# Kernel optimization log

Measured on AMD Instinct MI355X. Metric: run time of the kernel, lower is better.

The kernel has to match this reference:

```python
import jax, jax.numpy as jnp
import numpy as np
import math

NUM_HEADS = 16
HEAVY_RATIO = 0.1
RECENT_RATIO = 0.1
ROPE_THETA = 10000.0


def setup_inputs() -> dict:
    key = jax.random.key(0)
    ks = jax.random.split(key, 5)
    b, s, h = 1, 2048, 2048
    return {
        "hidden_states": jax.random.normal(ks[0], (b, s, h), dtype=jnp.float32),
        "Wq": jax.random.normal(ks[1], (h, h), dtype=jnp.float32) * 0.02,
        "Wk": jax.random.normal(ks[2], (h, h), dtype=jnp.float32) * 0.02,
        "Wv": jax.random.normal(ks[3], (h, h), dtype=jnp.float32) * 0.02,
        "Wo": jax.random.normal(ks[4], (h, h), dtype=jnp.float32) * 0.02,
    }


def _rotate_half(x):
    d = x.shape[-1]
    return jnp.concatenate([-x[..., d // 2:], x[..., : d // 2]], axis=-1)


def _rope(q, k, seq_len, head_dim, dtype):
    # LLaMA rotary embedding: inv_freq over even dims, emb = [freqs, freqs]
    inv_freq = 1.0 / (ROPE_THETA ** (jnp.arange(0, head_dim, 2, dtype=jnp.float32) / head_dim))
    pos = jnp.arange(seq_len, dtype=jnp.float32)
    freqs = pos[:, None] * inv_freq[None, :]            # [s, d/2]
    emb = jnp.concatenate([freqs, freqs], axis=-1)       # [s, d]
    cos = jnp.cos(emb).astype(dtype)[None, None]         # [1,1,s,d]
    sin = jnp.sin(emb).astype(dtype)[None, None]
    q = q * cos + _rotate_half(q) * sin
    k = k * cos + _rotate_half(k) * sin
    return q, k


def reference(hidden_states, Wq, Wk, Wv, Wo):
    b, s, hidden = hidden_states.shape
    H = NUM_HEADS
    d = hidden // H

    def proj(W):  # nn.Linear(x) = x @ W.T, then split heads -> [b,H,s,d]
        return (hidden_states @ W.T).reshape(b, s, H, d).transpose(0, 2, 1, 3)

    q, k, v = proj(Wq), proj(Wk), proj(Wv)
    q, k = _rope(q, k, s, d, hidden_states.dtype)

    scores = jnp.einsum("bhqd,bhkd->bhqk", q, k) / math.sqrt(d)  # [b,H,s,s]
    neg = jnp.finfo(scores.dtype).min
    i = jnp.arange(s)[:, None]
    j = jnp.arange(s)[None, :]
    causal = jnp.where(j <= i, jnp.array(0.0, scores.dtype), neg)
    scores = jnp.maximum(scores + causal, neg)

    heavy_budget = int(HEAVY_RATIO * s)
    recent_budget = int(RECENT_RATIO * s)

    # first softmax (fp32), accumulate column importances
    tmp_attn = jax.nn.softmax(scores.astype(jnp.float32), axis=-1).astype(scores.dtype)
    tmp_sum = jnp.sum(tmp_attn, axis=-2)                 # [b,H,s]
    _, topk_idx = jax.lax.top_k(tmp_sum, heavy_budget)   # [b,H,heavy]
    heavy_mask = jnp.any(topk_idx[..., :, None] == jnp.arange(s)[None, None, None, :], axis=-2)  # [b,H,s]

    # recent band: tril(diag=recent) & triu(diag=-recent)  <=>  |i-j| <= recent
    band = jnp.abs(i - j) <= recent_budget               # [s,s]
    mask = heavy_mask[:, :, None, :] | band[None, None]

    scores = jnp.where(mask, scores, neg)
    probs = jax.nn.softmax(scores.astype(jnp.float32), axis=-1).astype(q.dtype)
    attn = jnp.einsum("bhqk,bhkd->bhqd", probs, v)
    attn = attn.transpose(0, 2, 1, 3).reshape(b, s, hidden)
    return attn @ Wo.T
```

## Files before the change

kernel.cpp:

```cpp
#include <hip/hip_runtime.h>
#include <hip/hip_bf16.h>
#include <stdint.h>

#define SEQ   2048
#define HIDN  2048
#define NHEAD 16
#define HDIM  128
#define HEAVY 204
#define RECENT 204

typedef __attribute__((ext_vector_type(4))) float f32x4;
typedef __attribute__((ext_vector_type(8))) short bf16x8;
typedef unsigned short u16;
typedef unsigned int   u32;

static __device__ __forceinline__ u16 f2bf(float f){
  union { float f; u32 u; } v; v.f = f;
  u32 r = (v.u + 0x7FFFu + ((v.u >> 16) & 1u)) >> 16;
  return (u16)r;
}
static __device__ __forceinline__ float bf2f(u16 u){
  union { u32 u; float f; } v; v.u = ((u32)u) << 16;
  return v.f;
}

static __device__ __forceinline__ void gload16(const void* g, void* l){
  __builtin_amdgcn_global_load_lds((const __attribute__((address_space(1))) u32*)g,
                                   (__attribute__((address_space(3))) u32*)l, 16, 0, 0);
}

#define WAITVM(N) asm volatile("s_waitcnt vmcnt(" #N ")" ::: "memory")
#define BARRAW    __builtin_amdgcn_s_barrier()
#define PRIO1     __builtin_amdgcn_s_setprio(1)
#define PRIO0     __builtin_amdgcn_s_setprio(0)

static __device__ __forceinline__ void stage_tile(const u16* __restrict__ base, size_t stride,
                                                  int row0, u16* __restrict__ lds, int tid){
  const int wbase = tid & ~63;
#pragma unroll
  for (int it = 0; it < 4; ++it){
    int m = it * 256 + tid;
    int row = m >> 4, cp = m & 15;
    gload16(base + (size_t)(row0 + row) * stride + ((cp ^ (row & 7)) * 8),
            lds + (it * 256 + wbase) * 8);
  }
}

__global__ void k_prep(const float* __restrict__ A0, const float* __restrict__ A1,
                       const float* __restrict__ A2, const float* __restrict__ A3,
                       const float* __restrict__ A4, u16* __restrict__ out,
                       float* __restrict__ cosT, float* __restrict__ sinT,
                       float* __restrict__ colsum){
  int b = blockIdx.x, tid = threadIdx.x;
  if (b < 20480){
    int id = b * 256 + tid;
    int sel = id >> 20, off = (id & 1048575) * 4;
    const float* src = sel == 0 ? A0 : sel == 1 ? A1 : sel == 2 ? A2 : sel == 3 ? A3 : A4;
    float4 v = *(const float4*)(src + off);
    ushort4 o;
    o.x = f2bf(v.x); o.y = f2bf(v.y); o.z = f2bf(v.z); o.w = f2bf(v.w);
    *(ushort4*)(out + (size_t)sel * 4194304 + off) = o;
  } else if (b < 20992){
    int i = (b - 20480) * 256 + tid;
    int pos = i >> 6, j = i & 63;
    float invf = powf(10000.0f, -(float)j * (1.0f / 64.0f));
    float a = (float)pos * invf;
    cosT[i] = cosf(a);
    sinT[i] = sinf(a);
  } else {
    int i = (b - 20992) * 256 + tid;
    if (i < 16384) ((float4*)colsum)[i] = (float4){0.f, 0.f, 0.f, 0.f};
  }
}

__global__ void k_post(u16* __restrict__ Qm, u16* __restrict__ Km,
                       const float* __restrict__ cosT, const float* __restrict__ sinT,
                       const u16* __restrict__ V, u16* __restrict__ Vt){
  __shared__ u16 t[32][33];
  int b = blockIdx.x, tid = threadIdx.x;
  if (b < 4096){
    int gid = b * 256 + tid;
    u16* M = (gid < 524288) ? Qm : Km;
    int id = gid & 524287;
    int pos = id >> 8, rem = id & 255;
    int h = rem >> 4, j4 = (rem & 15) * 4;
    u16* p = M + (size_t)pos * HIDN + h * HDIM + j4;
    ushort4 lo = *(ushort4*)p;
    ushort4 hi = *(ushort4*)(p + 64);
    float4 c = *(const float4*)(cosT + pos * 64 + j4);
    float4 s = *(const float4*)(sinT + pos * 64 + j4);
    float l0 = bf2f(lo.x), l1 = bf2f(lo.y), l2 = bf2f(lo.z), l3 = bf2f(lo.w);
    float h0 = bf2f(hi.x), h1 = bf2f(hi.y), h2 = bf2f(hi.z), h3 = bf2f(hi.w);
    ushort4 nlo, nhi;
    nlo.x = f2bf(l0 * c.x - h0 * s.x);  nhi.x = f2bf(h0 * c.x + l0 * s.x);
    nlo.y = f2bf(l1 * c.y - h1 * s.y);  nhi.y = f2bf(h1 * c.y + l1 * s.y);
    nlo.z = f2bf(l2 * c.z - h2 * s.z);  nhi.z = f2bf(h2 * c.z + l2 * s.z);
    nlo.w = f2bf(l3 * c.w - h3 * s.w);  nhi.w = f2bf(h3 * c.w + l3 * s.w);
    *(ushort4*)p = nlo;
    *(ushort4*)(p + 64) = nhi;
  } else {
    int b2 = b - 4096;
    int s0 = (b2 & 63) * 32, c0 = (b2 >> 6) * 32;
    int r = tid >> 3, cc = (tid & 7) * 4;
    ushort4 v = *(const ushort4*)(V + (size_t)(s0 + r) * 2048 + c0 + cc);
    t[r][cc] = v.x; t[r][cc + 1] = v.y; t[r][cc + 2] = v.z; t[r][cc + 3] = v.w;
    __syncthreads();
    int co = tid >> 3, ro = (tid & 7) * 4;
    ushort4 o;
    o.x = t[ro][co]; o.y = t[ro + 1][co]; o.z = t[ro + 2][co]; o.w = t[ro + 3][co];
    *(ushort4*)(Vt + (size_t)(c0 + co) * 2048 + s0 + ro) = o;
  }
}

__global__ __launch_bounds__(512, 1)
void k_g256(const u16* __restrict__ X, const u16* __restrict__ Wq, const u16* __restrict__ Wk,
            const u16* __restrict__ Wv, u16* __restrict__ C0, u16* __restrict__ C1,
            u16* __restrict__ C2){
  __shared__ __align__(16) u16 LA[2][256 * 64];
  __shared__ __align__(16) u16 LB[2][192 * 64];
  const int tid = threadIdx.x;
  const int lane = tid & 63, wvi = tid >> 6;
  const int wm = wvi >> 2, wn = wvi & 3;
  const int g = lane >> 4, c15 = lane & 15;
  const int brow = blockIdx.y * 256;
  const int bcol = blockIdx.x * 192;
  const int NT = 32;

  f32x4 acc[8][3];
#pragma unroll
  for (int m = 0; m < 8; m++)
#pragma unroll
    for (int n = 0; n < 3; n++) acc[m][n] = (f32x4){0.f, 0.f, 0.f, 0.f};

  const int cc0 = ((g ^ (c15 & 7)) * 8);
  bf16x8 af[4][2], bf[3][2];

#define BPTR(rB_) (rB_ < 2048 ? Wq + (size_t)(rB_) * 2048 \
                 : rB_ < 4096 ? Wk + (size_t)((rB_) - 2048) * 2048 \
                              : Wv + (size_t)((rB_) - 4096) * 2048)
#define STGA(grow0, gcol0, ldsb) do { \
  _Pragma("unroll") for (int it = 0; it < 2; ++it){ \
    int m_ = it * 512 + tid; \
    int row_ = m_ >> 3, cp_ = m_ & 7; \
    gload16(X + (size_t)((grow0) + row_) * 2048 + (gcol0) + ((cp_ ^ (row_ & 7)) * 8), \
            (ldsb) + (it * 512 + (tid & ~63)) * 8); \
  } } while(0)
#define STGB128(gcol0, ldsb) do { \
  _Pragma("unroll") for (int it = 0; it < 2; ++it){ \
    int m_ = it * 512 + tid; \
    int row_ = m_ >> 3, cp_ = m_ & 7; \
    int rB_ = bcol + row_; \
    const u16* bp_ = BPTR(rB_); \
    gload16(bp_ + (gcol0) + ((cp_ ^ (row_ & 7)) * 8), \
            (ldsb) + (it * 512 + (tid & ~63)) * 8); \
  } } while(0)
#define STGB64(gcol0, ldsb) do { \
    int row_ = 128 + (tid >> 3), cp_ = tid & 7; \
    int rB_ = bcol + row_; \
    const u16* bp_ = BPTR(rB_); \
    gload16(bp_ + (gcol0) + ((cp_ ^ (row_ & 7)) * 8), \
            (ldsb) + (tid & ~63) * 8); \
  } while(0)
#define RDA(buf, mibase) \
  _Pragma("unroll") for (int mi2 = 0; mi2 < 4; ++mi2){ \
    const u16* pr = &LA[buf][0] + (size_t)(wm * 128 + ((mibase) + mi2) * 16 + c15) * 64; \
    af[mi2][0] = *(const bf16x8*)(pr + cc0); \
    af[mi2][1] = *(const bf16x8*)(pr + (cc0 ^ 32)); \
  }
#define RDB2(buf) \
  _Pragma("unroll") for (int ni2 = 0; ni2 < 2; ++ni2){ \
    const u16* pr = &LB[buf][0] + (size_t)(wn * 48 + ni2 * 16 + c15) * 64; \
    bf[ni2][0] = *(const bf16x8*)(pr + cc0); \
    bf[ni2][1] = *(const bf16x8*)(pr + (cc0 ^ 32)); \
  }
#define RDB1(buf) do { \
    const u16* pr = &LB[buf][0] + (size_t)(wn * 48 + 32 + c15) * 64; \
    bf[2][0] = *(const bf16x8*)(pr + cc0); \
    bf[2][1] = *(const bf16x8*)(pr + (cc0 ^ 32)); \
  } while(0)
#define MM2(mibase) \
  _Pragma("unroll") for (int mi2 = 0; mi2 < 4; ++mi2) \
  _Pragma("unroll") for (int ni2 = 0; ni2 < 2; ++ni2) \
  _Pragma("unroll") for (int kk = 0; kk < 2; ++kk) \
    acc[(mibase) + mi2][ni2] = __builtin_amdgcn_mfma_f32_16x16x32_bf16( \
        af[mi2][kk], bf[ni2][kk], acc[(mibase) + mi2][ni2], 0, 0, 0);
#define MM1(mibase) \
  _Pragma("unroll") for (int mi2 = 0; mi2 < 4; ++mi2) \
  _Pragma("unroll") for (int kk = 0; kk < 2; ++kk) \
    acc[(mibase) + mi2][2] = __builtin_amdgcn_mfma_f32_16x16x32_bf16( \
        af[mi2][kk], bf[2][kk], acc[(mibase) + mi2][2], 0, 0, 0);

  STGA(brow,       0, &LA[0][0]);
  STGA(brow + 128, 0, &LA[0][0] + 128 * 64);
  STGB128(0,  &LB[0][0]);
  STGB64(0,   &LB[0][0] + 128 * 64);
  STGB128(64, &LB[1][0]);
  STGB64(64,  &LB[1][0] + 128 * 64);
  WAITVM(3);
  BARRAW;

  for (int t = 0; t < NT; t += 2){
    const int kn1 = (t + 1) * 64;
    const int kn2 = (t + 2) * 64;
    const int kn3 = (t + 3) * 64;
    RDA(0, 0); RDB2(0);
    STGA(brow, kn1, &LA[1][0]);
    BARRAW; PRIO1; MM2(0); PRIO0; BARRAW;
    RDB1(0);
    STGA(brow + 128, kn1, &LA[1][0] + 128 * 64);
    BARRAW; PRIO1; MM1(0); PRIO0; BARRAW;
    RDA(0, 4);
    if (t + 2 < NT) STGB128(kn2, &LB[0][0]);
    BARRAW; PRIO1; MM1(4); PRIO0; BARRAW;
    if (t + 2 < NT){ STGB64(kn2, &LB[0][0] + 128 * 64); WAITVM(3); }
    else            { WAITVM(0); }
    BARRAW; PRIO1; MM2(4); PRIO0; BARRAW;
    RDA(1, 0); RDB2(1);
    if (t + 2 < NT) STGA(brow, kn2, &LA[0][0]);
    BARRAW; PRIO1; MM2(0); PRIO0; BARRAW;
    RDB1(1);
    if (t + 2 < NT) STGA(brow + 128, kn2, &LA[0][0] + 128 * 64);
    BARRAW; PRIO1; MM1(0); PRIO0; BARRAW;
    RDA(1, 4);
    if (t + 3 < NT) STGB128(kn3, &LB[1][0]);
    BARRAW; PRIO1; MM1(4); PRIO0; BARRAW;
    if (t + 3 < NT){ STGB64(kn3, &LB[1][0] + 128 * 64); WAITVM(3); }
    else if (t + 2 < NT){ WAITVM(0); }
    BARRAW; PRIO1; MM2(4); PRIO0; BARRAW;
  }
#undef BPTR
#undef STGA
#undef STGB128
#undef STGB64
#undef RDA
#undef RDB2
#undef RDB1
#undef MM2
#undef MM1

#pragma unroll
  for (int mi = 0; mi < 8; ++mi)
#pragma unroll
    for (int ni = 0; ni < 3; ++ni){
      int colbase = bcol + wn * 48 + ni * 16;
      int proj = colbase >> 11;
      u16* Cb = proj == 0 ? C0 : proj == 1 ? C1 : C2;
      int lc = (colbase & 2047) + c15;
#pragma unroll
      for (int r = 0; r < 4; ++r){
        int row = brow + wm * 128 + mi * 16 + g * 4 + r;
        Cb[(size_t)row * 2048 + lc] = f2bf(acc[mi][ni][r]);
      }
    }
}

static __device__ __forceinline__ void stage_g(const u16* __restrict__ A, const u16* __restrict__ B,
                                               int brow, int bcol, int k0,
                                               u16* __restrict__ as, u16* __restrict__ bs, int tid){
  const int wbase = tid & ~63;
#pragma unroll
  for (int it = 0; it < 2; ++it){
    int m = it * 256 + tid;
    int row = m >> 2, q = m & 3;
    gload16(A + (size_t)(brow + row) * 2048 + k0 + q * 8, as + (it * 256 + wbase) * 8);
    gload16(B + (size_t)(bcol + row) * 2048 + k0 + q * 8, bs + (it * 256 + wbase) * 8);
  }
}

__global__ __launch_bounds__(256)
void k_gemm_out(const u16* __restrict__ A, const u16* __restrict__ B, float* __restrict__ C){
  __shared__ __align__(16) u16 As[2][128 * 32];
  __shared__ __align__(16) u16 Bs[2][128 * 32];
  const int tid = threadIdx.x;
  const int w = tid >> 6, lane = tid & 63;
  const int wr = w >> 1, wc = w & 1;
  const int g = lane >> 4, c15 = lane & 15;
  const int brow = blockIdx.y * 128, bcol = blockIdx.x * 128;

  f32x4 acc[4][4];
#pragma unroll
  for (int m = 0; m < 4; m++)
#pragma unroll
    for (int n = 0; n < 4; n++) acc[m][n] = (f32x4){0.f, 0.f, 0.f, 0.f};

  stage_g(A, B, brow, bcol, 0, As[0], Bs[0], tid);
  int cur = 0;
  for (int kt = 0; kt < 64; ++kt){
    if (kt + 1 < 64){ stage_g(A, B, brow, bcol, (kt + 1) * 32, As[cur ^ 1], Bs[cur ^ 1], tid);
                      WAITVM(4); }
    else            { WAITVM(0); }
    BARRAW;
    bf16x8 af[4], bfr[4];
#pragma unroll
    for (int m = 0; m < 4; m++) af[m] = *(const bf16x8*)(As[cur] + (wr * 64 + m * 16 + c15) * 32 + g * 8);
#pragma unroll
    for (int n = 0; n < 4; n++) bfr[n] = *(const bf16x8*)(Bs[cur] + (wc * 64 + n * 16 + c15) * 32 + g * 8);
    PRIO1;
#pragma unroll
    for (int m = 0; m < 4; m++)
#pragma unroll
      for (int n = 0; n < 4; n++)
        acc[m][n] = __builtin_amdgcn_mfma_f32_16x16x32_bf16(af[m], bfr[n], acc[m][n], 0, 0, 0);
    PRIO0;
    BARRAW;
    cur ^= 1;
  }
#pragma unroll
  for (int m = 0; m < 4; m++)
#pragma unroll
    for (int n = 0; n < 4; n++)
#pragma unroll
      for (int r = 0; r < 4; r++){
        int row = brow + wr * 64 + m * 16 + g * 4 + r;
        int col = bcol + wc * 64 + n * 16 + c15;
        C[(size_t)row * 2048 + col] = acc[m][n][r];
      }
}

__global__ __launch_bounds__(256)
void k_pass1a(const u16* __restrict__ Q, const u16* __restrict__ K, float* __restrict__ rowsum){
  __shared__ __align__(16) u16 Ks[2][64 * 128];
  const int tid = threadIdx.x;
  const int wv = tid >> 6, lane = tid & 63;
  const int g = lane >> 4, c15 = lane & 15;
  const int h = blockIdx.y;
  int qb = 0, c = 0;
  { int rem = blockIdx.x; int q = 0;
    while (rem >= ((2 * q + 9) >> 3)){ rem -= (2 * q + 9) >> 3; q++; }
    qb = q; c = rem; }
  const int i0 = qb * 128;
  const int ktend = 2 * qb + 2;
  const int kt0 = c * 8;
  const int kt1 = (ktend < kt0 + 8) ? ktend : (kt0 + 8);
  const u16* Qh = Q + h * HDIM;
  const u16* Kh = K + h * HDIM;
  const float scale = 0.08838834764831845f;
  const int wb = wv * 32;

  bf16x8 qfr[2][4];
#pragma unroll
  for (int m = 0; m < 2; m++)
#pragma unroll
    for (int ks = 0; ks < 4; ks++)
      qfr[m][ks] = *(const bf16x8*)(Qh + (size_t)(i0 + wb + m * 16 + c15) * 2048 + ks * 32 + g * 8);

  stage_tile(Kh, 2048, kt0 * 64, Ks[0], tid);

  float rs[2][4] = {{0.f,0.f,0.f,0.f},{0.f,0.f,0.f,0.f}};
  int cur = 0;
  for (int kt = kt0; kt < kt1; ++kt){
    if (kt + 1 < kt1){ stage_tile(Kh, 2048, (kt + 1) * 64, Ks[cur ^ 1], tid); WAITVM(4); }
    else             { WAITVM(0); }
    BARRAW;
    const int k0 = kt * 64;
    f32x4 sacc[2][4];
#pragma unroll
    for (int m = 0; m < 2; m++)
#pragma unroll
      for (int n = 0; n < 4; n++) sacc[m][n] = (f32x4){0.f, 0.f, 0.f, 0.f};
#pragma unroll
    for (int ks = 0; ks < 4; ++ks){
#pragma unroll
      for (int n = 0; n < 4; n++){
        int brw = n * 16 + c15;
        bf16x8 b = *(const bf16x8*)(Ks[cur] + brw * 128 + ((ks * 32 + g * 8) ^ ((brw & 7) << 3)));
#pragma unroll
        for (int m = 0; m < 2; m++)
          sacc[m][n] = __builtin_amdgcn_mfma_f32_16x16x32_bf16(qfr[m][ks], b, sacc[m][n], 0, 0, 0);
      }
    }
    if (kt < 2 * qb){
#pragma unroll
      for (int m = 0; m < 2; m++)
#pragma unroll
        for (int n = 0; n < 4; n++)
#pragma unroll
          for (int r = 0; r < 4; r++)
            rs[m][r] += __expf(sacc[m][n][r] * scale);
    } else {
#pragma unroll
      for (int n = 0; n < 4; n++){
        int col = k0 + n * 16 + c15;
#pragma unroll
        for (int m = 0; m < 2; m++)
#pragma unroll
          for (int r = 0; r < 4; r++){
            int rowg = i0 + wb + m * 16 + g * 4 + r;
            rs[m][r] += (col <= rowg) ? __expf(sacc[m][n][r] * scale) : 0.f;
          }
      }
    }
    BARRAW;
    cur ^= 1;
  }
#pragma unroll
  for (int m = 0; m < 2; m++)
#pragma unroll
    for (int r = 0; r < 4; r++){
      float v = rs[m][r];
      v += __shfl_xor(v, 1); v += __shfl_xor(v, 2);
      v += __shfl_xor(v, 4); v += __shfl_xor(v, 8);
      if (c15 == 0)
        atomicAdd(&rowsum[h * 2048 + i0 + wb + m * 16 + g * 4 + r], v);
    }
}

__global__ __launch_bounds__(256)
void k_pass1b(const u16* __restrict__ Q, const u16* __restrict__ K,
              const float* __restrict__ rowsum, float* __restrict__ colsum){
  __shared__ __align__(16) u16 Qs[2][64 * 128];
  const int tid = threadIdx.x;
  const int wv = tid >> 6, lane = tid & 63;
  const int g = lane >> 4, c15 = lane & 15;
  const int h = blockIdx.y;
  int kb = 0, c = 0;
  { int rem = blockIdx.x; int q = 0;
    while (rem >= ((39 - 2 * q) >> 3)){ rem -= (39 - 2 * q) >> 3; q++; }
    kb = q; c = rem; }
  const int k0 = kb * 128;
  const int qt0 = 2 * kb + c * 8;
  const int qt1 = (2 * kb + c * 8 + 8 < 32) ? (2 * kb + c * 8 + 8) : 32;
  const u16* Qh = Q + h * HDIM;
  const u16* Kh = K + h * HDIM;
  const float scale = 0.08838834764831845f;
  const int wb = wv * 32;
  const float* rsrow = rowsum + h * 2048;

  bf16x8 kfr[2][4];
#pragma unroll
  for (int m = 0; m < 2; m++)
#pragma unroll
    for (int ks = 0; ks < 4; ks++)
      kfr[m][ks] = *(const bf16x8*)(Kh + (size_t)(k0 + wb + m * 16 + c15) * 2048 + ks * 32 + g * 8);

  stage_tile(Qh, 2048, qt0 * 64, Qs[0], tid);

  float racc[2][4] = {{0.f,0.f,0.f,0.f},{0.f,0.f,0.f,0.f}};
  int cur = 0;
  for (int qt = qt0; qt < qt1; ++qt){
    if (qt + 1 < qt1){ stage_tile(Qh, 2048, (qt + 1) * 64, Qs[cur ^ 1], tid); WAITVM(4); }
    else             { WAITVM(0); }
    BARRAW;
    const int i0q = qt * 64;
    float rw[4];
#pragma unroll
    for (int n = 0; n < 4; n++)
      rw[n] = 1.0f / rsrow[i0q + n * 16 + c15];
    f32x4 sacc[2][4];
#pragma unroll
    for (int m = 0; m < 2; m++)
#pragma unroll
      for (int n = 0; n < 4; n++) sacc[m][n] = (f32x4){0.f, 0.f, 0.f, 0.f};
#pragma unroll
    for (int ks = 0; ks < 4; ++ks){
#pragma unroll
      for (int n = 0; n < 4; n++){
        int brw = n * 16 + c15;
        bf16x8 b = *(const bf16x8*)(Qs[cur] + brw * 128 + ((ks * 32 + g * 8) ^ ((brw & 7) << 3)));
#pragma unroll
        for (int m = 0; m < 2; m++)
          sacc[m][n] = __builtin_amdgcn_mfma_f32_16x16x32_bf16(kfr[m][ks], b, sacc[m][n], 0, 0, 0);
      }
    }
    if (qt >= 2 * kb + 2){
#pragma unroll
      for (int m = 0; m < 2; m++)
#pragma unroll
        for (int n = 0; n < 4; n++)
#pragma unroll
          for (int r = 0; r < 4; r++)
            racc[m][r] += __expf(sacc[m][n][r] * scale) * rw[n];
    } else {
#pragma unroll
      for (int n = 0; n < 4; n++){
        int colq = i0q + n * 16 + c15;
#pragma unroll
        for (int m = 0; m < 2; m++)
#pragma unroll
          for (int r = 0; r < 4; r++){
            int rowk = k0 + wb + m * 16 + g * 4 + r;
            racc[m][r] += (rowk <= colq) ? __expf(sacc[m][n][r] * scale) * rw[n] : 0.f;
          }
      }
    }
    BARRAW;
    cur ^= 1;
  }
#pragma unroll
  for (int m = 0; m < 2; m++)
#pragma unroll
    for (int r = 0; r < 4; r++){
      float v = racc[m][r];
      v += __shfl_xor(v, 1); v += __shfl_xor(v, 2);
      v += __shfl_xor(v, 4); v += __shfl_xor(v, 8);
      if (c15 == 0)
        atomicAdd(&colsum[h * 2048 + k0 + wb + m * 16 + g * 4 + r], v);
    }
}

__global__ __launch_bounds__(1024)
void k_topk(const float* __restrict__ colsum, short* __restrict__ cidx){
  __shared__ float v[2048];
  __shared__ short ix[2048];
  __shared__ short sx[256];
  const int tid = threadIdx.x;
  const int h = blockIdx.x;
  for (int i = tid; i < 2048; i += 1024){ v[i] = colsum[h * 2048 + i]; ix[i] = (short)i; }
  __syncthreads();
  for (int k = 2; k <= 2048; k <<= 1){
    for (int j = k >> 1; j > 0; j >>= 1){
      int i = ((tid / j) * (j << 1)) + (tid % j);
      int l = i + j;
      float vi = v[i], vl = v[l];
      short ii = ix[i], il = ix[l];
      bool before_i = (vi > vl) || (vi == vl && ii < il);
      bool dir = (i & k) == 0;
      if (dir ? !before_i : before_i){ v[i] = vl; v[l] = vi; ix[i] = il; ix[l] = ii; }
      __syncthreads();
    }
  }
  if (tid < 256) sx[tid] = (tid < HEAVY) ? ix[tid] : (short)32767;
  __syncthreads();
  for (int k = 2; k <= 256; k <<= 1){
    for (int j = k >> 1; j > 0; j >>= 1){
      if (tid < 128){
        int i = ((tid / j) * (j << 1)) + (tid % j);
        int l = i + j;
        short a = sx[i], b = sx[l];
        bool asc = (i & k) == 0;
        if (asc ? (a > b) : (a < b)){ sx[i] = b; sx[l] = a; }
      }
      __syncthreads();
    }
  }
  if (tid < 256) cidx[h * 256 + tid] = sx[tid];
}

__global__ void k_gatherKV(const u16* __restrict__ Kb, const u16* __restrict__ Vb,
                           const short* __restrict__ cidx,
                           u16* __restrict__ Kg, u16* __restrict__ Vg){
  __shared__ __align__(16) u16 t[32][136];
  int b = blockIdx.x, tid = threadIdx.x;
  if (b < 256){
    int gid = b * 256 + tid;
    int h = gid >> 12, rem = gid & 4095;
    int slot = rem >> 4, cp = rem & 15;
    int cid = cidx[h * 256 + slot];
    bf16x8 z = (bf16x8){0,0,0,0,0,0,0,0};
    bf16x8 val = (cid < 2048) ? *(const bf16x8*)(Kb + (size_t)cid * 2048 + h * 128 + cp * 8) : z;
    *(bf16x8*)(Kg + ((size_t)h * 256 + slot) * 128 + cp * 8) = val;
  } else {
    int b2 = b - 256;
    int h = b2 >> 3, s0 = (b2 & 7) * 32;
#pragma unroll
    for (int it = 0; it < 2; ++it){
      int m = it * 256 + tid;
      int s = m >> 4, cp = m & 15;
      int cid = cidx[h * 256 + s0 + s];
      bf16x8 z = (bf16x8){0,0,0,0,0,0,0,0};
      bf16x8 val = (cid < 2048) ? *(const bf16x8*)(Vb + (size_t)cid * 2048 + h * 128 + cp * 8) : z;
      *(bf16x8*)(&t[s][cp * 8]) = val;
    }
    __syncthreads();
#pragma unroll
    for (int i = 0; i < 16; ++i){
      int idx = i * 256 + tid;
      int d = idx >> 5, s = idx & 31;
      Vg[((size_t)h * 128 + d) * 256 + s0 + s] = t[s][d];
    }
  }
}

static __device__ __forceinline__ void load_vf(const u16* __restrict__ Vt,
                                               const u16* __restrict__ Vg,
                                               int h, int e, int g, int c15,
                                               bf16x8 vf[2][8]){
  const bool isg = (e >= 100);
#pragma unroll
  for (int ks2 = 0; ks2 < 2; ++ks2)
#pragma unroll
    for (int f = 0; f < 8; ++f){
      int vrow = f * 16 + c15;
      vf[ks2][f] = isg
        ? *(const bf16x8*)(Vg + ((size_t)h * 128 + vrow) * 256 + (e - 100) * 64 + ks2 * 32 + g * 8)
        : *(const bf16x8*)(Vt + ((size_t)h * 128 + vrow) * 2048 + e * 64 + ks2 * 32 + g * 8);
    }
}

__global__ __launch_bounds__(256)
void k_pass2(const u16* __restrict__ Q, const u16* __restrict__ K, const u16* __restrict__ Vt,
             const u16* __restrict__ Kg, const u16* __restrict__ Vg,
             const short* __restrict__ cidx, u16* __restrict__ attn){
  __shared__ __align__(16) u16 Qs[64 * 128];
  __shared__ __align__(16) u16 Ks[2][64 * 128];
  __shared__ __align__(16) u16 Ps[4][16 * 64];
  __shared__ short cids[256];
  __shared__ int lists[12];
  __shared__ int nact_s;
  const int tid = threadIdx.x;
  const int w = tid >> 6, lane = tid & 63;
  const int g = lane >> 4, c15 = lane & 15;
  const int qb = blockIdx.x, h = blockIdx.y;
  const int i0 = qb * 64;
  const u16* Qh = Q + h * HDIM;
  const u16* Kh = K + h * HDIM;
  const u16* Kgh = Kg + (size_t)h * 256 * 128;
  const float scale = 0.08838834764831845f;
  const int arow = w * 16 + c15;

  if (tid < 256) cids[tid] = cidx[h * 256 + tid];
  __syncthreads();
  if (tid == 0){
    int n = 0;
    int ktb0 = (i0 > RECENT) ? ((i0 - RECENT) >> 6) : 0;
    for (int kt = ktb0; kt <= qb; ++kt) lists[n++] = kt;
    for (int gt = 0; gt < 4; ++gt)
      if ((int)cids[gt * 64] <= i0 - RECENT + 62) lists[n++] = 100 + gt;
    nact_s = n;
  }
  __syncthreads();
  const int nact = nact_s;

  stage_tile(Qh, 2048, i0, Qs, tid);
  { int e = lists[0];
    if (e < 100) stage_tile(Kh, 2048, e * 64, Ks[0], tid);
    else         stage_tile(Kgh, 128, (e - 100) * 64, Ks[0], tid); }
  bf16x8 vf[2][8];
  load_vf(Vt, Vg, h, lists[0], g, c15, vf);
  WAITVM(16);
  BARRAW;

  f32x4 oacc[8];
#pragma unroll
  for (int f = 0; f < 8; f++) oacc[f] = (f32x4){0.f, 0.f, 0.f, 0.f};
  float lsum[4] = {0.f, 0.f, 0.f, 0.f};

  int cur = 0;
  for (int i = 0; i < nact; ++i){
    const int e = lists[i];
    const bool isg = (e >= 100);
    const bool nxt = (i + 1 < nact);
    if (nxt){
      int e2 = lists[i + 1];
      if (e2 < 100) stage_tile(Kh, 2048, e2 * 64, Ks[cur ^ 1], tid);
      else          stage_tile(Kgh, 128, (e2 - 100) * 64, Ks[cur ^ 1], tid);
      WAITVM(20);
    } else {
      WAITVM(16);
    }
    BARRAW;
    f32x4 sacc[4];
#pragma unroll
    for (int n = 0; n < 4; n++) sacc[n] = (f32x4){0.f, 0.f, 0.f, 0.f};
#pragma unroll
    for (int ks = 0; ks < 4; ++ks){
      bf16x8 a = *(const bf16x8*)(Qs + arow * 128 + ((ks * 32 + g * 8) ^ ((arow & 7) << 3)));
#pragma unroll
      for (int n = 0; n < 4; n++){
        int brw = n * 16 + c15;
        bf16x8 b = *(const bf16x8*)(Ks[cur] + brw * 128 + ((ks * 32 + g * 8) ^ ((brw & 7) << 3)));
        sacc[n] = __builtin_amdgcn_mfma_f32_16x16x32_bf16(a, b, sacc[n], 0, 0, 0);
      }
    }
#pragma unroll
    for (int n = 0; n < 4; n++){
      int cid = isg ? (int)cids[(e - 100) * 64 + n * 16 + c15] : (e * 64 + n * 16 + c15);
#pragma unroll
      for (int r = 0; r < 4; r++){
        int rowg = i0 + w * 16 + g * 4 + r;
        int dist = rowg - cid;
        bool valid = (cid <= rowg) && (isg ? (dist > RECENT) : (dist <= RECENT));
        float ev = valid ? __expf(sacc[n][r] * scale) : 0.f;
        lsum[r] += ev;
        int prow = g * 4 + r;
        Ps[w][prow * 64 + ((n * 16 + c15) ^ ((prow & 7) << 3))] = f2bf(ev);
      }
    }
    if (nxt) WAITVM(4); else WAITVM(0);
    PRIO1;
#pragma unroll
    for (int ks2 = 0; ks2 < 2; ++ks2){
      bf16x8 pa = *(const bf16x8*)(&Ps[w][c15 * 64 + ((ks2 * 32 + g * 8) ^ ((c15 & 7) << 3))]);
#pragma unroll
      for (int f = 0; f < 8; ++f)
        oacc[f] = __builtin_amdgcn_mfma_f32_16x16x32_bf16(pa, vf[ks2][f], oacc[f], 0, 0, 0);
    }
    PRIO0;
    if (nxt) load_vf(Vt, Vg, h, lists[i + 1], g, c15, vf);
    BARRAW;
    cur ^= 1;
  }
  float rinv[4];
#pragma unroll
  for (int r = 0; r < 4; r++){
    float v = lsum[r];
    v += __shfl_xor(v, 1); v += __shfl_xor(v, 2);
    v += __shfl_xor(v, 4); v += __shfl_xor(v, 8);
    rinv[r] = 1.0f / v;
  }
#pragma unroll
  for (int f = 0; f < 8; f++)
#pragma unroll
    for (int r = 0; r < 4; r++){
      int rowg = i0 + w * 16 + g * 4 + r;
      attn[(size_t)rowg * 2048 + h * HDIM + f * 16 + c15] = f2bf(oacc[f][r] * rinv[r]);
    }
}

extern "C" void kernel_launch(void* const* d_in, const int* in_sizes, int n_in,
                              void* d_out, int out_size, void* d_ws, size_t ws_size,
                              hipStream_t stream){
  const float* X  = (const float*)d_in[0];
  const float* Wq = (const float*)d_in[1];
  const float* Wk = (const float*)d_in[2];
  const float* Wv = (const float*)d_in[3];
  const float* Wo = (const float*)d_in[4];

  char* w = (char*)d_ws;
  const size_t MB8 = (size_t)2048 * 2048 * 2;
  u16* Xb  = (u16*)(w);
  u16* Wqb = (u16*)(w + 1 * MB8);
  u16* Wkb = (u16*)(w + 2 * MB8);
  u16* Wvb = (u16*)(w + 3 * MB8);
  u16* Wob = (u16*)(w + 4 * MB8);
  u16* Qb  = (u16*)(w + 5 * MB8);
  u16* Kb  = (u16*)(w + 6 * MB8);
  u16* Vb  = (u16*)(w + 7 * MB8);
  u16* Vtb   = Wqb;
  u16* attnb = Xb;
  char* p = w + 8 * MB8;
  float* cosT = (float*)p;              p += 524288;
  float* sinT = (float*)p;              p += 524288;
  float* colsum = (float*)p;            p += 131072;
  float* rowsum = (float*)p;            p += 131072;
  short* cidx  = (short*)p;             p += 16 * 256 * 2;
  u16*   Kg    = (u16*)p;               p += (size_t)16 * 256 * 128 * 2;
  u16*   Vg    = (u16*)p;

  dim3 b256(256);

  k_prep<<<21056, b256, 0, stream>>>(X, Wq, Wk, Wv, Wo, Xb, cosT, sinT, colsum);

  k_g256<<<dim3(32, 8), dim3(512), 0, stream>>>(Xb, Wqb, Wkb, Wvb, Qb, Kb, Vb);
  k_post<<<8192, b256, 0, stream>>>(Qb, Kb, cosT, sinT, Vb, Vtb);

  k_pass1a<<<dim3(40, 16), b256, 0, stream>>>(Qb, Kb, rowsum);
  k_pass1b<<<dim3(40, 16), b256, 0, stream>>>(Qb, Kb, rowsum, colsum);
  k_topk<<<16, dim3(1024), 0, stream>>>(colsum, cidx);
  k_gatherKV<<<384, b256, 0, stream>>>(Kb, Vb, cidx, Kg, Vg);
  k_pass2<<<dim3(32, 16), b256, 0, stream>>>(Qb, Kb, Vtb, Kg, Vg, cidx, attnb);

  k_gemm_out<<<dim3(16, 16), b256, 0, stream>>>(attnb, Wob, (float*)d_out);
}
```

Baseline: 262.4 us.

## Radix-select topk fused with KV gather; wider pass2 and output GEMM tiles

```diff
diff --git a/kernel.cpp b/kernel.cpp
--- a/kernel.cpp
+++ b/kernel.cpp
@@ -43,6 +43,27 @@
     int row = m >> 4, cp = m & 15;
     gload16(base + (size_t)(row0 + row) * stride + ((cp ^ (row & 7)) * 8),
             lds + (it * 256 + wbase) * 8);
+  }
+}
+
+static __device__ __forceinline__ void stageK512(const u16* __restrict__ base, size_t stride,
+                                                 int row0, u16* __restrict__ lds, int tid){
+#pragma unroll
+  for (int it = 0; it < 2; ++it){
+    int m = it * 512 + tid;
+    int row = m >> 4, cp = m & 15;
+    gload16(base + (size_t)(row0 + row) * stride + ((cp ^ (row & 7)) * 8),
+            lds + (it * 512 + (tid & ~63)) * 8);
+  }
+}
+static __device__ __forceinline__ void stageV512(const u16* __restrict__ base, size_t stride,
+                                                 int c0, u16* __restrict__ lds, int tid){
+#pragma unroll
+  for (int it = 0; it < 2; ++it){
+    int m = it * 512 + tid;
+    int row = m >> 3, cp = m & 7;
+    gload16(base + (size_t)row * stride + c0 + ((cp ^ (row & 7)) * 8),
+            lds + (it * 512 + (tid & ~63)) * 8);
   }
 }
 
@@ -254,66 +275,75 @@
     }
 }
 
-static __device__ __forceinline__ void stage_g(const u16* __restrict__ A, const u16* __restrict__ B,
-                                               int brow, int bcol, int k0,
-                                               u16* __restrict__ as, u16* __restrict__ bs, int tid){
-  const int wbase = tid & ~63;
-#pragma unroll
-  for (int it = 0; it < 2; ++it){
-    int m = it * 256 + tid;
-    int row = m >> 2, q = m & 3;
-    gload16(A + (size_t)(brow + row) * 2048 + k0 + q * 8, as + (it * 256 + wbase) * 8);
-    gload16(B + (size_t)(bcol + row) * 2048 + k0 + q * 8, bs + (it * 256 + wbase) * 8);
-  }
-}
-
-__global__ __launch_bounds__(256)
+__global__ __launch_bounds__(512)
 void k_gemm_out(const u16* __restrict__ A, const u16* __restrict__ B, float* __restrict__ C){
-  __shared__ __align__(16) u16 As[2][128 * 32];
-  __shared__ __align__(16) u16 Bs[2][128 * 32];
+  __shared__ __align__(16) u16 As[2][128 * 64];
+  __shared__ __align__(16) u16 Bs[2][128 * 64];
   const int tid = threadIdx.x;
   const int w = tid >> 6, lane = tid & 63;
-  const int wr = w >> 1, wc = w & 1;
+  const int wm = w >> 1, wn = w & 1;
   const int g = lane >> 4, c15 = lane & 15;
   const int brow = blockIdx.y * 128, bcol = blockIdx.x * 128;
-
-  f32x4 acc[4][4];
-#pragma unroll
-  for (int m = 0; m < 4; m++)
+  const int cc0 = ((g ^ (c15 & 7)) * 8);
+
+  f32x4 acc[2][4];
+#pragma unroll
+  for (int m = 0; m < 2; m++)
 #pragma unroll
     for (int n = 0; n < 4; n++) acc[m][n] = (f32x4){0.f, 0.f, 0.f, 0.f};
 
-  stage_g(A, B, brow, bcol, 0, As[0], Bs[0], tid);
+#define STG_O(k0, buf) do { \
+  _Pragma("unroll") for (int it = 0; it < 2; ++it){ \
+    int m_ = it * 512 + tid; \
+    int row_ = m_ >> 3, cp_ = m_ & 7; \
+    gload16(A + (size_t)(brow + row_) * 2048 + (k0) + ((cp_ ^ (row_ & 7)) * 8), \
+            As[buf] + (it * 512 + (tid & ~63)) * 8); \
+    gload16(B + (size_t)(bcol + row_) * 2048 + (k0) + ((cp_ ^ (row_ & 7)) * 8), \
+            Bs[buf] + (it * 512 + (tid & ~63)) * 8); \
+  } } while(0)
+
+  STG_O(0, 0);
   int cur = 0;
-  for (int kt = 0; kt < 64; ++kt){
-    if (kt + 1 < 64){ stage_g(A, B, brow, bcol, (kt + 1) * 32, As[cur ^ 1], Bs[cur ^ 1], tid);
-                      WAITVM(4); }
+  for (int kt = 0; kt < 32; ++kt){
+    if (kt + 1 < 32){ STG_O((kt + 1) * 64, cur ^ 1); WAITVM(4); }
     else            { WAITVM(0); }
     BARRAW;
-    bf16x8 af[4], bfr[4];
-#pragma unroll
-    for (int m = 0; m < 4; m++) af[m] = *(const bf16x8*)(As[cur] + (wr * 64 + m * 16 + c15) * 32 + g * 8);
-#pragma unroll
-    for (int n = 0; n < 4; n++) bfr[n] = *(const bf16x8*)(Bs[cur] + (wc * 64 + n * 16 + c15) * 32 + g * 8);
+    bf16x8 af[2][2], bfr[4][2];
+#pragma unroll
+    for (int mi = 0; mi < 2; ++mi){
+      const u16* pr = As[cur] + (size_t)(wm * 32 + mi * 16 + c15) * 64;
+      af[mi][0] = *(const bf16x8*)(pr + cc0);
+      af[mi][1] = *(const bf16x8*)(pr + (cc0 ^ 32));
+    }
+#pragma unroll
+    for (int ni = 0; ni < 4; ++ni){
+      const u16* pr = Bs[cur] + (size_t)(wn * 64 + ni * 16 + c15) * 64;
+      bfr[ni][0] = *(const bf16x8*)(pr + cc0);
+      bfr[ni][1] = *(const bf16x8*)(pr + (cc0 ^ 32));
+    }
     PRIO1;
 #pragma unroll
-    for (int m = 0; m < 4; m++)
-#pragma unroll
-      for (int n = 0; n < 4; n++)
-        acc[m][n] = __builtin_amdgcn_mfma_f32_16x16x32_bf16(af[m], bfr[n], acc[m][n], 0, 0, 0);
+    for (int mi = 0; mi < 2; ++mi)
+#pragma unroll
+      for (int ni = 0; ni < 4; ++ni)
+#pragma unroll
+        for (int kk = 0; kk < 2; ++kk)
+          acc[mi][ni] = __builtin_amdgcn_mfma_f32_16x16x32_bf16(af[mi][kk], bfr[ni][kk],
+                                                                acc[mi][ni], 0, 0, 0);
     PRIO0;
     BARRAW;
     cur ^= 1;
   }
-#pragma unroll
-  for (int m = 0; m < 4; m++)
-#pragma unroll
-    for (int n = 0; n < 4; n++)
-#pragma unroll
-      for (int r = 0; r < 4; r++){
-        int row = brow + wr * 64 + m * 16 + g * 4 + r;
-        int col = bcol + wc * 64 + n * 16 + c15;
-        C[(size_t)row * 2048 + col] = acc[m][n][r];
+#undef STG_O
+#pragma unroll
+  for (int mi = 0; mi < 2; ++mi)
+#pragma unroll
+    for (int ni = 0; ni < 4; ++ni)
+#pragma unroll
+      for (int r = 0; r < 4; ++r){
+        int row = brow + wm * 32 + mi * 16 + g * 4 + r;
+        int col = bcol + wn * 64 + ni * 16 + c15;
+        C[(size_t)row * 2048 + col] = acc[mi][ni][r];
       }
 }
 
@@ -499,101 +529,112 @@
 }
 
 __global__ __launch_bounds__(1024)
-void k_topk(const float* __restrict__ colsum, short* __restrict__ cidx){
-  __shared__ float v[2048];
-  __shared__ short ix[2048];
-  __shared__ short sx[256];
+void k_topkg(const float* __restrict__ colsum, const u16* __restrict__ Kb,
+             const u16* __restrict__ Vb, short* __restrict__ cidx,
+             u16* __restrict__ Kg, u16* __restrict__ Vg){
+  __shared__ u32 keys[2048];
+  __shared__ int hist[256];
+  __shared__ int chunkCnt[32];
+  __shared__ short cidL[256];
+  __shared__ u32 Tacc_s;
+  __shared__ int rem_s;
+  __shared__ __align__(16) u16 t[32][136];
   const int tid = threadIdx.x;
   const int h = blockIdx.x;
-  for (int i = tid; i < 2048; i += 1024){ v[i] = colsum[h * 2048 + i]; ix[i] = (short)i; }
+  const int w = tid >> 6, lane = tid & 63;
+
+  for (int i = tid; i < 2048; i += 1024) keys[i] = ((const u32*)colsum)[h * 2048 + i];
+  if (tid == 0){ Tacc_s = 0; rem_s = HEAVY; }
   __syncthreads();
-  for (int k = 2; k <= 2048; k <<= 1){
-    for (int j = k >> 1; j > 0; j >>= 1){
-      int i = ((tid / j) * (j << 1)) + (tid % j);
-      int l = i + j;
-      float vi = v[i], vl = v[l];
-      short ii = ix[i], il = ix[l];
-      bool before_i = (vi > vl) || (vi == vl && ii < il);
-      bool dir = (i & k) == 0;
-      if (dir ? !before_i : before_i){ v[i] = vl; v[l] = vi; ix[i] = il; ix[l] = ii; }
-      __syncthreads();
-    }
-  }
-  if (tid < 256) sx[tid] = (tid < HEAVY) ? ix[tid] : (short)32767;
+
+  for (int s = 24; s >= 0; s -= 8){
+    if (tid < 256) hist[tid] = 0;
+    __syncthreads();
+    u32 T = Tacc_s;
+    for (int i = tid; i < 2048; i += 1024){
+      u32 k = keys[i];
+      bool match = (s == 24) ? true : (((k ^ T) >> (s + 8)) == 0);
+      if (match) atomicAdd(&hist[(k >> s) & 255], 1);
+    }
+    __syncthreads();
+    if (tid == 0){
+      int rem = rem_s, acc = 0, b = 255;
+      for (; b > 0; --b){
+        int c2 = hist[b];
+        if (acc + c2 >= rem) break;
+        acc += c2;
+      }
+      Tacc_s = T | ((u32)b << s);
+      rem_s = rem - acc;
+    }
+    __syncthreads();
+  }
+  const u32 T = Tacc_s;
+  const int need = rem_s;
+  const u32 kA = keys[tid], kB = keys[tid + 1024];
+  const bool eqA = (kA == T), eqB = (kB == T);
+  unsigned long long ebA = __ballot(eqA);
+  unsigned long long ebB = __ballot(eqB);
+  if (lane == 0){ chunkCnt[w] = __popcll(ebA); chunkCnt[16 + w] = __popcll(ebB); }
   __syncthreads();
-  for (int k = 2; k <= 256; k <<= 1){
-    for (int j = k >> 1; j > 0; j >>= 1){
-      if (tid < 128){
-        int i = ((tid / j) * (j << 1)) + (tid % j);
-        int l = i + j;
-        short a = sx[i], b = sx[l];
-        bool asc = (i & k) == 0;
-        if (asc ? (a > b) : (a < b)){ sx[i] = b; sx[l] = a; }
-      }
-      __syncthreads();
-    }
-  }
-  if (tid < 256) cidx[h * 256 + tid] = sx[tid];
-}
-
-__global__ void k_gatherKV(const u16* __restrict__ Kb, const u16* __restrict__ Vb,
-                           const short* __restrict__ cidx,
-                           u16* __restrict__ Kg, u16* __restrict__ Vg){
-  __shared__ __align__(16) u16 t[32][136];
-  int b = blockIdx.x, tid = threadIdx.x;
-  if (b < 256){
-    int gid = b * 256 + tid;
-    int h = gid >> 12, rem = gid & 4095;
-    int slot = rem >> 4, cp = rem & 15;
-    int cid = cidx[h * 256 + slot];
+  if (tid == 0){
+    int s2 = 0;
+    for (int i2 = 0; i2 < 32; ++i2){ int c2 = chunkCnt[i2]; chunkCnt[i2] = s2; s2 += c2; }
+  }
+  __syncthreads();
+  const unsigned long long below = (1ull << lane) - 1ull;
+  const int eqrA = chunkCnt[w] + __popcll(ebA & below);
+  const int eqrB = chunkCnt[16 + w] + __popcll(ebB & below);
+  const bool hvA = (kA > T) || (eqA && eqrA < need);
+  const bool hvB = (kB > T) || (eqB && eqrB < need);
+  __syncthreads();
+  unsigned long long hbA = __ballot(hvA);
+  unsigned long long hbB = __ballot(hvB);
+  if (lane == 0){ chunkCnt[w] = __popcll(hbA); chunkCnt[16 + w] = __popcll(hbB); }
+  if (tid >= HEAVY && tid < 256) cidL[tid] = 32767;
+  __syncthreads();
+  if (tid == 0){
+    int s2 = 0;
+    for (int i2 = 0; i2 < 32; ++i2){ int c2 = chunkCnt[i2]; chunkCnt[i2] = s2; s2 += c2; }
+  }
+  __syncthreads();
+  if (hvA) cidL[chunkCnt[w] + __popcll(hbA & below)] = (short)tid;
+  if (hvB) cidL[chunkCnt[16 + w] + __popcll(hbB & below)] = (short)(tid + 1024);
+  __syncthreads();
+  if (tid < 256) cidx[h * 256 + tid] = cidL[tid];
+
+  for (int i = tid; i < 4096; i += 1024){
+    int slot = i >> 4, cp = i & 15;
+    int cid = cidL[slot];
     bf16x8 z = (bf16x8){0,0,0,0,0,0,0,0};
     bf16x8 val = (cid < 2048) ? *(const bf16x8*)(Kb + (size_t)cid * 2048 + h * 128 + cp * 8) : z;
     *(bf16x8*)(Kg + ((size_t)h * 256 + slot) * 128 + cp * 8) = val;
-  } else {
-    int b2 = b - 256;
-    int h = b2 >> 3, s0 = (b2 & 7) * 32;
-#pragma unroll
-    for (int it = 0; it < 2; ++it){
-      int m = it * 256 + tid;
-      int s = m >> 4, cp = m & 15;
-      int cid = cidx[h * 256 + s0 + s];
+  }
+  for (int grp = 0; grp < 8; ++grp){
+    int s0 = grp * 32;
+    if (tid < 512){
+      int s2 = tid >> 4, cp = tid & 15;
+      int cid = cidL[s0 + s2];
       bf16x8 z = (bf16x8){0,0,0,0,0,0,0,0};
       bf16x8 val = (cid < 2048) ? *(const bf16x8*)(Vb + (size_t)cid * 2048 + h * 128 + cp * 8) : z;
-      *(bf16x8*)(&t[s][cp * 8]) = val;
+      *(bf16x8*)(&t[s2][cp * 8]) = val;
     }
     __syncthreads();
-#pragma unroll
-    for (int i = 0; i < 16; ++i){
-      int idx = i * 256 + tid;
-      int d = idx >> 5, s = idx & 31;
-      Vg[((size_t)h * 128 + d) * 256 + s0 + s] = t[s][d];
-    }
-  }
-}
-
-static __device__ __forceinline__ void load_vf(const u16* __restrict__ Vt,
-                                               const u16* __restrict__ Vg,
-                                               int h, int e, int g, int c15,
-                                               bf16x8 vf[2][8]){
-  const bool isg = (e >= 100);
-#pragma unroll
-  for (int ks2 = 0; ks2 < 2; ++ks2)
-#pragma unroll
-    for (int f = 0; f < 8; ++f){
-      int vrow = f * 16 + c15;
-      vf[ks2][f] = isg
-        ? *(const bf16x8*)(Vg + ((size_t)h * 128 + vrow) * 256 + (e - 100) * 64 + ks2 * 32 + g * 8)
-        : *(const bf16x8*)(Vt + ((size_t)h * 128 + vrow) * 2048 + e * 64 + ks2 * 32 + g * 8);
-    }
-}
-
-__global__ __launch_bounds__(256)
+    for (int i = tid; i < 4096; i += 1024){
+      int d = i >> 5, s2 = i & 31;
+      Vg[((size_t)h * 128 + d) * 256 + s0 + s2] = t[s2][d];
+    }
+    __syncthreads();
+  }
+}
+
+__global__ __launch_bounds__(512)
 void k_pass2(const u16* __restrict__ Q, const u16* __restrict__ K, const u16* __restrict__ Vt,
              const u16* __restrict__ Kg, const u16* __restrict__ Vg,
              const short* __restrict__ cidx, u16* __restrict__ attn){
-  __shared__ __align__(16) u16 Qs[64 * 128];
   __shared__ __align__(16) u16 Ks[2][64 * 128];
-  __shared__ __align__(16) u16 Ps[4][16 * 64];
+  __shared__ __align__(16) u16 Vs[2][128 * 64];
+  __shared__ __align__(16) u16 Ps[8][16 * 64];
   __shared__ short cids[256];
   __shared__ int lists[12];
   __shared__ int nact_s;
@@ -601,33 +642,40 @@
   const int w = tid >> 6, lane = tid & 63;
   const int g = lane >> 4, c15 = lane & 15;
   const int qb = blockIdx.x, h = blockIdx.y;
-  const int i0 = qb * 64;
+  const int i0 = qb * 128;
+  const int wq = w >> 2, w4 = w & 3;
+  const int rowbase = i0 + wq * 64 + w4 * 16;
   const u16* Qh = Q + h * HDIM;
   const u16* Kh = K + h * HDIM;
   const u16* Kgh = Kg + (size_t)h * 256 * 128;
+  const u16* Vth = Vt + (size_t)h * 128 * 2048;
+  const u16* Vgh = Vg + (size_t)h * 128 * 256;
   const float scale = 0.08838834764831845f;
-  const int arow = w * 16 + c15;
 
   if (tid < 256) cids[tid] = cidx[h * 256 + tid];
+  bf16x8 qfr[4];
+#pragma unroll
+  for (int ks = 0; ks < 4; ks++)
+    qfr[ks] = *(const bf16x8*)(Qh + (size_t)(rowbase + c15) * 2048 + ks * 32 + g * 8);
   __syncthreads();
   if (tid == 0){
     int n = 0;
     int ktb0 = (i0 > RECENT) ? ((i0 - RECENT) >> 6) : 0;
-    for (int kt = ktb0; kt <= qb; ++kt) lists[n++] = kt;
+    int ktmax = (i0 + 127) >> 6;
+    for (int kt = ktb0; kt <= ktmax; ++kt) lists[n++] = kt;
     for (int gt = 0; gt < 4; ++gt)
-      if ((int)cids[gt * 64] <= i0 - RECENT + 62) lists[n++] = 100 + gt;
+      if ((int)cids[gt * 64] <= i0 + 127 - RECENT - 1) lists[n++] = 100 + gt;
     nact_s = n;
   }
   __syncthreads();
   const int nact = nact_s;
 
-  stage_tile(Qh, 2048, i0, Qs, tid);
   { int e = lists[0];
-    if (e < 100) stage_tile(Kh, 2048, e * 64, Ks[0], tid);
-    else         stage_tile(Kgh, 128, (e - 100) * 64, Ks[0], tid); }
-  bf16x8 vf[2][8];
-  load_vf(Vt, Vg, h, lists[0], g, c15, vf);
-  WAITVM(16);
+    if (e < 100){ stageK512(Kh, 2048, e * 64, Ks[0], tid);
+                  stageV512(Vth, 2048, e * 64, Vs[0], tid); }
+    else        { stageK512(Kgh, 128, (e - 100) * 64, Ks[0], tid);
+                  stageV512(Vgh, 256, (e - 100) * 64, Vs[0], tid); } }
+  WAITVM(2);
   BARRAW;
 
   f32x4 oacc[8];
@@ -642,11 +690,13 @@
     const bool nxt = (i + 1 < nact);
     if (nxt){
       int e2 = lists[i + 1];
-      if (e2 < 100) stage_tile(Kh, 2048, e2 * 64, Ks[cur ^ 1], tid);
-      else          stage_tile(Kgh, 128, (e2 - 100) * 64, Ks[cur ^ 1], tid);
-      WAITVM(20);
+      if (e2 < 100){ stageK512(Kh, 2048, e2 * 64, Ks[cur ^ 1], tid);
+                     stageV512(Vth, 2048, e2 * 64, Vs[cur ^ 1], tid); }
+      else         { stageK512(Kgh, 128, (e2 - 100) * 64, Ks[cur ^ 1], tid);
+                     stageV512(Vgh, 256, (e2 - 100) * 64, Vs[cur ^ 1], tid); }
+      WAITVM(6);
     } else {
-      WAITVM(16);
+      WAITVM(2);
     }
     BARRAW;
     f32x4 sacc[4];
@@ -654,12 +704,11 @@
     for (int n = 0; n < 4; n++) sacc[n] = (f32x4){0.f, 0.f, 0.f, 0.f};
 #pragma unroll
     for (int ks = 0; ks < 4; ++ks){
-      bf16x8 a = *(const bf16x8*)(Qs + arow * 128 + ((ks * 32 + g * 8) ^ ((arow & 7) << 3)));
 #pragma unroll
       for (int n = 0; n < 4; n++){
         int brw = n * 16 + c15;
         bf16x8 b = *(const bf16x8*)(Ks[cur] + brw * 128 + ((ks * 32 + g * 8) ^ ((brw & 7) << 3)));
-        sacc[n] = __builtin_amdgcn_mfma_f32_16x16x32_bf16(a, b, sacc[n], 0, 0, 0);
+        sacc[n] = __builtin_amdgcn_mfma_f32_16x16x32_bf16(qfr[ks], b, sacc[n], 0, 0, 0);
       }
     }
 #pragma unroll
@@ -667,7 +716,7 @@
       int cid = isg ? (int)cids[(e - 100) * 64 + n * 16 + c15] : (e * 64 + n * 16 + c15);
 #pragma unroll
       for (int r = 0; r < 4; r++){
-        int rowg = i0 + w * 16 + g * 4 + r;
+        int rowg = rowbase + g * 4 + r;
         int dist = rowg - cid;
         bool valid = (cid <= rowg) && (isg ? (dist > RECENT) : (dist <= RECENT));
         float ev = valid ? __expf(sacc[n][r] * scale) : 0.f;
@@ -677,16 +726,19 @@
       }
     }
     if (nxt) WAITVM(4); else WAITVM(0);
+    BARRAW;
     PRIO1;
 #pragma unroll
     for (int ks2 = 0; ks2 < 2; ++ks2){
       bf16x8 pa = *(const bf16x8*)(&Ps[w][c15 * 64 + ((ks2 * 32 + g * 8) ^ ((c15 & 7) << 3))]);
 #pragma unroll
-      for (int f = 0; f < 8; ++f)
-        oacc[f] = __builtin_amdgcn_mfma_f32_16x16x32_bf16(pa, vf[ks2][f], oacc[f], 0, 0, 0);
+      for (int f = 0; f < 8; ++f){
+        int vrow = f * 16 + c15;
+        bf16x8 vb = *(const bf16x8*)(Vs[cur] + vrow * 64 + ((ks2 * 32 + g * 8) ^ ((vrow & 7) << 3)));
+        oacc[f] = __builtin_amdgcn_mfma_f32_16x16x32_bf16(pa, vb, oacc[f], 0, 0, 0);
+      }
     }
     PRIO0;
-    if (nxt) load_vf(Vt, Vg, h, lists[i + 1], g, c15, vf);
     BARRAW;
     cur ^= 1;
   }
@@ -702,7 +754,7 @@
   for (int f = 0; f < 8; f++)
 #pragma unroll
     for (int r = 0; r < 4; r++){
-      int rowg = i0 + w * 16 + g * 4 + r;
+      int rowg = rowbase + g * 4 + r;
       attn[(size_t)rowg * 2048 + h * HDIM + f * 16 + c15] = f2bf(oacc[f][r] * rinv[r]);
     }
 }
@@ -746,9 +798,8 @@
 
   k_pass1a<<<dim3(40, 16), b256, 0, stream>>>(Qb, Kb, rowsum);
   k_pass1b<<<dim3(40, 16), b256, 0, stream>>>(Qb, Kb, rowsum, colsum);
-  k_topk<<<16, dim3(1024), 0, stream>>>(colsum, cidx);
-  k_gatherKV<<<384, b256, 0, stream>>>(Kb, Vb, cidx, Kg, Vg);
-  k_pass2<<<dim3(32, 16), b256, 0, stream>>>(Qb, Kb, Vtb, Kg, Vg, cidx, attnb);
-
-  k_gemm_out<<<dim3(16, 16), b256, 0, stream>>>(attnb, Wob, (float*)d_out);
-}
+  k_topkg<<<16, dim3(1024), 0, stream>>>(colsum, Kb, Vb, cidx, Kg, Vg);
+  k_pass2<<<dim3(16, 16), dim3(512), 0, stream>>>(Qb, Kb, Vtb, Kg, Vg, cidx, attnb);
+
+  k_gemm_out<<<dim3(16, 16), dim3(512), 0, stream>>>(attnb, Wob, (float*)d_out);
+}
```

Result: faster. 246.9 us (-5.9%).
